# Kernel optimization log

Measured on AMD Instinct MI355X. Metric: run time of the kernel, lower is better.

The kernel has to match this reference:

```python
import jax, jax.numpy as jnp
import numpy as np

B, N, D, DFC, EMB, L = 16, 1024, 128, 128, 64, 4
NHOPS = (1, 2, 3, 4)  # tatic='cont': nhop(i) = i + 1
EDGE_P = 0.03


def _make_adj(k):
    u = jax.random.uniform(k, (B, N, N))
    a = u < EDGE_P
    a = a | jnp.transpose(a, (0, 2, 1))          # undirected
    a = a | jnp.eye(N, dtype=bool)[None]         # self loops
    return a.astype(jnp.float32)


def setup_inputs() -> dict:
    key = jax.random.key(0)
    ks = jax.random.split(key, 16)
    s = 0.05
    x = jax.random.normal(ks[0], (B, N, 2 * EMB), jnp.float32)
    adj1 = _make_adj(ks[1])
    adj2 = _make_adj(ks[2])
    valid = jnp.ones((B, N), jnp.float32)
    embede_w = jax.random.normal(ks[3], (D, 2 * EMB)) * s
    gW = jax.random.normal(ks[4], (L, D, D)) * s
    gb = jnp.zeros((L, D), jnp.float32)
    gA = jax.random.normal(ks[5], (L, D, D)) * s
    gate_w = jax.random.normal(ks[6], (L, 1, 2 * D)) * s
    gate_b = jnp.zeros((L, 1), jnp.float32)
    fc0_w = jax.random.normal(ks[7], (DFC, D)) * s
    fc0_b = jnp.zeros((DFC,), jnp.float32)
    fc1_w = jax.random.normal(ks[8], (DFC, DFC)) * s
    fc1_b = jnp.zeros((DFC,), jnp.float32)
    fc2_w = jax.random.normal(ks[9], (DFC, DFC)) * s
    fc2_b = jnp.zeros((DFC,), jnp.float32)
    fc3_w = jax.random.normal(ks[10], (1, DFC)) * s
    fc3_b = jnp.zeros((1,), jnp.float32)
    return dict(x=x, adj1=adj1, adj2=adj2, valid=valid, embede_w=embede_w,
                gW=gW, gb=gb, gA=gA, gate_w=gate_w, gate_b=gate_b,
                fc0_w=fc0_w, fc0_b=fc0_b, fc1_w=fc1_w, fc1_b=fc1_b,
                fc2_w=fc2_w, fc2_b=fc2_b, fc3_w=fc3_w, fc3_b=fc3_b)


def _glema(x, adj, W, b, A, gw, gbias, nhop):
    h = x @ W.T + b                                        # [B,N,D]
    e = jnp.einsum('bjl,bkl->bjk', jnp.einsum('bjd,de->bje', h, A), h)
    e = e + jnp.transpose(e, (0, 2, 1))                    # undirected
    att = jnp.where(adj > 0, e, jnp.float32(0.0))
    att = jax.nn.softmax(att, axis=1) * adj                # softmax over dim 1, then adj mask
    az = jax.nn.relu(jnp.einsum('bij,bjd->bid', att, h))
    coeff = jax.nn.sigmoid(jnp.concatenate([h, az], -1) @ gw.T + gbias)  # [B,N,1]
    z = h
    for _ in range(nhop):
        az = jax.nn.relu(jnp.einsum('bij,bjd->bid', att, z))
        z = coeff * h + (1.0 - coeff) * az
    return z


def reference(x, adj1, adj2, valid, embede_w, gW, gb, gA, gate_w, gate_b,
              fc0_w, fc0_b, fc1_w, fc1_b, fc2_w, fc2_b, fc3_w, fc3_b):
    h = x @ embede_w.T                                     # embede (no bias)
    for k in range(L):                                     # branch='both': c_hs2 - c_hs1
        h1 = _glema(h, adj1, gW[k], gb[k], gA[k], gate_w[k], gate_b[k], NHOPS[k])
        h2 = _glema(h, adj2, gW[k], gb[k], gA[k], gate_w[k], gate_b[k], NHOPS[k])
        h = h2 - h1                                        # dropout p used in eval mode -> identity
    h = h * valid[..., None]
    pooled = h.sum(1) / valid.sum(1, keepdims=True)        # [B,D]
    y = jax.nn.relu(pooled @ fc0_w.T + fc0_b)
    y = jax.nn.relu(y @ fc1_w.T + fc1_b)
    y = jax.nn.relu(y @ fc2_w.T + fc2_b)
    y = jax.nn.sigmoid(y @ fc3_w.T + fc3_b)
    return y.reshape(-1)                                   # [B]
```

## Files before the change

kernel.cpp:

```cpp
#include <hip/hip_runtime.h>

typedef _Float16 half_t;
typedef _Float16 half8 __attribute__((ext_vector_type(8)));
typedef _Float16 half4v __attribute__((ext_vector_type(4)));
typedef float floatx4 __attribute__((ext_vector_type(4)));

#define MFMA(a,b,c) __builtin_amdgcn_mfma_f32_16x16x32_f16(a,b,c,0,0,0)

#define NB 16
#define NLEN 1024
#define DD 128
#define BN (NB*NLEN)
#define BND ((size_t)NB*NLEN*DD)
#define BNN ((size_t)NB*NLEN*NLEN)
#define ELLS 128
#define EMP 1044

static __device__ inline half_t f16h(unsigned pk) {
    unsigned short us = (unsigned short)(pk & 0xffffu);
    half_t h; __builtin_memcpy(&h, &us, 2); return h;
}

__global__ __launch_bounds__(256, 8)
void k_pre(const float* __restrict__ adj1, const float* __restrict__ adj2,
           unsigned* __restrict__ ell, unsigned* __restrict__ cntA,
           const float* __restrict__ x, const float* __restrict__ Ew, half_t* __restrict__ h16,
           const float* __restrict__ gW, const float* __restrict__ gA,
           half_t* __restrict__ Wf, half_t* __restrict__ STf) {
    int tid = threadIdx.x;
    int bid = blockIdx.x;
    if (bid < 8192) {
        int w = tid >> 6, l = tid & 63;
        int R = bid * 4 + w;
        int br = R >> 14, nb = R & 16383;
        const float* arow = (br ? adj2 : adj1) + (size_t)nb * 1024;
        float4 v0 = *(const float4*)&arow[l * 4];
        float4 v1 = *(const float4*)&arow[256 + l * 4];
        float4 v2 = *(const float4*)&arow[512 + l * 4];
        float4 v3 = *(const float4*)&arow[768 + l * 4];
        unsigned m = 0u;
        m |= (v0.x > 0.f) ? 1u : 0u;        m |= (v0.y > 0.f) ? 2u : 0u;
        m |= (v0.z > 0.f) ? 4u : 0u;        m |= (v0.w > 0.f) ? 8u : 0u;
        m |= (v1.x > 0.f) ? 0x10u : 0u;     m |= (v1.y > 0.f) ? 0x20u : 0u;
        m |= (v1.z > 0.f) ? 0x40u : 0u;     m |= (v1.w > 0.f) ? 0x80u : 0u;
        m |= (v2.x > 0.f) ? 0x100u : 0u;    m |= (v2.y > 0.f) ? 0x200u : 0u;
        m |= (v2.z > 0.f) ? 0x400u : 0u;    m |= (v2.w > 0.f) ? 0x800u : 0u;
        m |= (v3.x > 0.f) ? 0x1000u : 0u;   m |= (v3.y > 0.f) ? 0x2000u : 0u;
        m |= (v3.z > 0.f) ? 0x4000u : 0u;   m |= (v3.w > 0.f) ? 0x8000u : 0u;
        int cnt = __popc(m);
        int pre = cnt;
#pragma unroll
        for (int off = 1; off < 64; off <<= 1) {
            int o = __shfl_up(pre, off);
            if (l >= off) pre += o;
        }
        int total = __shfl(pre, 63);
        int idx = pre - cnt;
        unsigned* erow = ell + (size_t)R * ELLS;
        unsigned mm = m;
        while (mm) {
            int i = __builtin_ctz(mm);
            mm &= mm - 1;
            if (idx < ELLS)
                erow[idx] = ((unsigned)(((i >> 2) << 8) + l * 4 + (i & 3))) << 16;
            idx++;
        }
        int cnc = total > ELLS ? ELLS : total;
        if (l == 0) cntA[R] = (unsigned)cnc;
        if (l < 4 && cnc + l < ELLS) erow[cnc + l] = 0u;
        return;
    }
    if (bid >= 10240) {
        int i = (bid - 10240) * 256 + tid;
        Wf[i] = (half_t)gW[i];
        int base = i & ~16383;
        int lrem = i & 16383;
        int d = lrem >> 7, e = lrem & 127;
        STf[base + (e << 7) + d] = (half_t)(gA[i] + gA[base + (e << 7) + d]);
        return;
    }
    __shared__ float rows[8][DD];
    int g = (bid - 8192) * 8;
    {
        int nl = tid >> 5, c4 = (tid & 31) * 4;
        *(float4*)&rows[nl][c4] = *(const float4*)&x[(size_t)(g + nl) * DD + c4];
    }
    __syncthreads();
    int t = tid & 127, half = tid >> 7;
    const float4* wr4 = (const float4*)(Ew + (size_t)t * DD);
    float acc[4] = {0.f, 0.f, 0.f, 0.f};
#pragma unroll 4
    for (int k4 = 0; k4 < 32; k4++) {
        float4 wv = wr4[k4];
#pragma unroll
        for (int mi = 0; mi < 4; mi++) {
            float4 rv = *(const float4*)&rows[half + 2 * mi][k4 * 4];
            acc[mi] += rv.x * wv.x + rv.y * wv.y + rv.z * wv.z + rv.w * wv.w;
        }
    }
#pragma unroll
    for (int mi = 0; mi < 4; mi++) h16[(size_t)(g + half + 2 * mi) * DD + t] = (half_t)acc[mi];
}

__global__ __launch_bounds__(256)
void k_proj(const half_t* __restrict__ pa, const half_t* __restrict__ pb,
            const half_t* __restrict__ Wf, const float* __restrict__ bias,
            const half_t* __restrict__ STf,
            half_t* __restrict__ hbr16, half_t* __restrict__ hbrF, half_t* __restrict__ hSF) {
    __shared__ half_t htile[32 * 136];
    __shared__ half_t hbtile[32 * 136];
    int g = blockIdx.x * 32;
    int t = threadIdx.x;
    int w = t >> 6, l = t & 63, q = l >> 4, l15 = l & 15;
#pragma unroll
    for (int v = 0; v < 2; v++) {
        int idx = v * 256 + t; int r = idx >> 4, c8 = (idx & 15) * 8;
        half8 va = *(const half8*)&pa[((size_t)(g + r) << 7) + c8];
        if (pb) {
            half8 vb = *(const half8*)&pb[((size_t)(g + r) << 7) + c8];
            va = va - vb;
        }
        *(half8*)&htile[r * 136 + c8] = va;
    }
    __syncthreads();
    int rowh = (w & 1) * 16;
    int c0 = (w >> 1) * 4;
    half8 a1[4];
#pragma unroll
    for (int kc = 0; kc < 4; kc++) a1[kc] = *(const half8*)&htile[(rowh + l15) * 136 + kc * 32 + q * 8];
    floatx4 acc[4];
#pragma unroll
    for (int cc = 0; cc < 4; cc++) {
        int col = (c0 + cc) * 16 + l15;
        floatx4 a = {0.f, 0.f, 0.f, 0.f};
#pragma unroll
        for (int kc = 0; kc < 4; kc++) {
            half8 bf = *(const half8*)&Wf[((size_t)col << 7) + kc * 32 + q * 8];
            a = MFMA(a1[kc], bf, a);
        }
        float bv = bias[col];
        a.x += bv; a.y += bv; a.z += bv; a.w += bv;
        acc[cc] = a;
    }
#pragma unroll
    for (int cc = 0; cc < 4; cc++) {
        int col = (c0 + cc) * 16 + l15;
#pragma unroll
        for (int r = 0; r < 4; r++)
            hbtile[(rowh + q * 4 + r) * 136 + col] = (half_t)acc[cc][r];
    }
    __syncthreads();
    half8 a2[4];
#pragma unroll
    for (int kc = 0; kc < 4; kc++) a2[kc] = *(const half8*)&hbtile[(rowh + l15) * 136 + kc * 32 + q * 8];
#pragma unroll
    for (int cc = 0; cc < 4; cc++) {
        int col = (c0 + cc) * 16 + l15;
        floatx4 a = {0.f, 0.f, 0.f, 0.f};
#pragma unroll
        for (int kc = 0; kc < 4; kc++) {
            half8 bf = *(const half8*)&STf[((size_t)col << 7) + kc * 32 + q * 8];
            a = MFMA(a2[kc], bf, a);
        }
        acc[cc] = a;
    }
    __syncthreads();
#pragma unroll
    for (int cc = 0; cc < 4; cc++) {
        int col = (c0 + cc) * 16 + l15;
#pragma unroll
        for (int r = 0; r < 4; r++) htile[(rowh + q * 4 + r) * 136 + col] = (half_t)acc[cc][r];
    }
    __syncthreads();
#pragma unroll
    for (int v = 0; v < 2; v++) {
        int idx = v * 256 + t; int r = idx >> 4, c8 = (idx & 15) * 8;
        *(half8*)&hbr16[((size_t)(g + r) << 7) + c8] = *(const half8*)&hbtile[r * 136 + c8];
    }
#pragma unroll
    for (int v = 0; v < 2; v++) {
        int fi = v * 256 + t;
        int g2 = fi >> 8, kc = (fi >> 6) & 3, li = fi & 63;
        int src = (g2 * 16 + (li & 15)) * 136 + kc * 32 + (li >> 4) * 8;
        size_t dst = (((size_t)(blockIdx.x * 2 + g2) * 4 + kc) << 10) + li * 8;
        *(half8*)&hbrF[dst] = *(const half8*)&hbtile[src];
        *(half8*)&hSF[dst]  = *(const half8*)&htile[src];
    }
}

__global__ __launch_bounds__(256)
void k_E(const half_t* __restrict__ hSF, const half_t* __restrict__ hbrF,
         const half_t* __restrict__ hbr16,
         unsigned* __restrict__ ell, const unsigned* __restrict__ cntA,
         float* __restrict__ rsr, half_t* __restrict__ hbrs) {
    int hw = blockIdx.y * 64 + blockIdx.x;
    int wk = (hw & 7) * 128 + (hw >> 3);
    int b = wk >> 6, s = wk & 63;
    int t = threadIdx.x, w = t >> 6, l = t & 63, q = l >> 4, l15 = l & 15;
    __shared__ half_t emS[16 * EMP];
    __shared__ float rsS[2][16];
    size_t Gb = (size_t)b * 64;
    half8 A[4];
#pragma unroll
    for (int kc = 0; kc < 4; kc++)
        A[kc] = *(const half8*)&hSF[(((Gb + s) * 4 + kc) << 10) + l * 8];
#pragma unroll 4
    for (int cg = 0; cg < 16; cg++) {
        int c0 = w * 256 + cg * 16;
        floatx4 a = {0.f, 0.f, 0.f, 0.f};
#pragma unroll
        for (int kc = 0; kc < 4; kc++) {
            half8 bf = *(const half8*)&hbrF[(((Gb + w * 16 + cg) * 4 + kc) << 10) + l * 8];
            a = MFMA(A[kc], bf, a);
        }
#pragma unroll
        for (int r = 0; r < 4; r++)
            emS[(q * 4 + r) * EMP + c0 + l15] = (half_t)a[r];
    }
    __syncthreads();
    const float CN = 0.000335462627903f;
#pragma unroll
    for (int rr = 0; rr < 4; rr++) {
        int rl = w * 4 + rr;
        int rowg = b * 1024 + s * 16 + rl;
#pragma unroll
        for (int br = 0; br < 2; br++) {
            size_t R = ((size_t)br << 14) + rowg;
            int cn = (int)cntA[R];
            float rs = 0.f;
            for (int base = 0; base < cn; base += 64) {
                int si = base + l;
                float v = 0.f;
                if (si < cn) {
                    unsigned pk = ell[R * ELLS + si];
                    int col = (int)(pk >> 16);
                    float em = (float)emS[rl * EMP + col];
                    v = __expf(em - 8.f);
                    half_t hv = (half_t)v;
                    unsigned short us; __builtin_memcpy(&us, &hv, 2);
                    ((unsigned short*)ell)[(R * ELLS + si) * 2] = us;
                }
                rs += v;
            }
            rs += __shfl_xor(rs, 1); rs += __shfl_xor(rs, 2);
            rs += __shfl_xor(rs, 4); rs += __shfl_xor(rs, 8);
            rs += __shfl_xor(rs, 16); rs += __shfl_xor(rs, 32);
            if (l == 0) {
                float rv = 1.f / (rs + (1024.f - (float)cn) * CN);
                rsr[R] = rv;
                rsS[br][rl] = rv;
            }
        }
    }
    __syncthreads();
    const half_t* hrow = hbr16 + ((size_t)b << 17) + ((size_t)(s * 16) << 7);
#pragma unroll
    for (int v = 0; v < 2; v++) {
        int idx = v * 256 + t;
        int row = idx >> 5, br2 = (idx >> 4) & 1, ch = idx & 15;
        half8 hv = *(const half8*)&hrow[(size_t)row * 128 + ch * 8];
        float sc = rsS[br2][row];
        half8 o;
#pragma unroll
        for (int d = 0; d < 8; d++) o[d] = (half_t)(sc * (float)hv[d]);
        *(half8*)&hbrs[(size_t)br2 * BND + ((size_t)(b * 1024 + s * 16 + row) << 7) + ch * 8] = o;
    }
}

__global__ __launch_bounds__(256)
void k_az(const unsigned* __restrict__ ell, const unsigned* __restrict__ cntA,
          const float* __restrict__ rsr,
          const half_t* __restrict__ zin, const half_t* __restrict__ hbr16,
          const float* __restrict__ gw, const float* __restrict__ gb_,
          float* __restrict__ cfb, half_t* __restrict__ outp, int mode) {
    int t = threadIdx.x, w = t >> 6, l = t & 63;
    int g = l >> 4, l15 = l & 15;
    int bid = blockIdx.x;
    int wk = (bid & 7) * 256 + (bid >> 3);
    int R = wk * 16 + w * 4 + g;
    int br = R >> 14, nb = R & 16383;
    const unsigned* ep = ell + (size_t)R * ELLS;
    int cn = (int)cntA[R];
    const half_t* zb = zin + (size_t)br * BND + (((size_t)(nb & ~1023)) << 7) + l15 * 8;
    half8 acc8a = {}, acc8b = {};
    uint4 p4 = *(const uint4*)ep;
    for (int s = 0; s < cn; s += 4) {
        uint4 cur = p4;
        p4 = *(const uint4*)(ep + s + 4);
        half8 z0 = *(const half8*)(zb + (((size_t)(cur.x >> 16)) << 7));
        half8 z1 = *(const half8*)(zb + (((size_t)(cur.y >> 16)) << 7));
        half8 z2 = *(const half8*)(zb + (((size_t)(cur.z >> 16)) << 7));
        half8 z3 = *(const half8*)(zb + (((size_t)(cur.w >> 16)) << 7));
        half_t h0 = f16h(cur.x), h1 = f16h(cur.y), h2 = f16h(cur.z), h3 = f16h(cur.w);
        half8 s0 = {h0,h0,h0,h0,h0,h0,h0,h0};
        half8 s1 = {h1,h1,h1,h1,h1,h1,h1,h1};
        half8 s2 = {h2,h2,h2,h2,h2,h2,h2,h2};
        half8 s3 = {h3,h3,h3,h3,h3,h3,h3,h3};
        acc8a += z0 * s0;
        acc8b += z1 * s1;
        acc8a += z2 * s2;
        acc8b += z3 * s3;
    }
    float acc[8];
#pragma unroll
    for (int d = 0; d < 8; d++) acc[d] = fmaxf((float)acc8a[d] + (float)acc8b[d], 0.f);
    half8 hv8 = *(const half8*)&hbr16[((size_t)nb << 7) + l15 * 8];
    float hv[8];
#pragma unroll
    for (int d = 0; d < 8; d++) hv[d] = (float)hv8[d];
    float cf;
    if (mode >= 3) {
        const float* g1 = gw + l15 * 8;
        const float* g2 = gw + 128 + l15 * 8;
        float dp = 0.f;
#pragma unroll
        for (int d = 0; d < 8; d++) dp += hv[d] * g1[d] + acc[d] * g2[d];
        dp += __shfl_xor(dp, 1); dp += __shfl_xor(dp, 2);
        dp += __shfl_xor(dp, 4); dp += __shfl_xor(dp, 8);
        cf = 1.f / (1.f + __expf(-(dp + gb_[0])));
        if (l15 == 0) cfb[R] = cf;
    } else {
        cf = cfb[R];
    }
    float sc = (mode == 1 || mode == 3) ? rsr[R] : 1.f;
    half8 o;
#pragma unroll
    for (int d = 0; d < 8; d++)
        o[d] = (half_t)(sc * (cf * hv[d] + (1.f - cf) * acc[d]));
    *(half8*)&outp[(size_t)R * DD + l15 * 8] = o;
}

__global__ __launch_bounds__(256)
void k_pool(const half_t* __restrict__ z2, const half_t* __restrict__ z1,
            const float* __restrict__ valid, float* __restrict__ part) {
    int b = blockIdx.y, s = blockIdx.x;
    int t = threadIdx.x, d = t & 127, hf = t >> 7;
    __shared__ float red[128];
    float acc = 0.f;
    int nbase = s * 128 + hf * 64;
    for (int n = nbase; n < nbase + 64; n++) {
        size_t gi = ((size_t)(b * 1024 + n) << 7) + d;
        acc += ((float)z2[gi] - (float)z1[gi]) * valid[b * 1024 + n];
    }
    if (hf) red[d] = acc;
    __syncthreads();
    if (!hf) part[(b * 8 + s) * 128 + d] = acc + red[d];
}

__global__ __launch_bounds__(128)
void k_mlp(const float* __restrict__ part, const float* __restrict__ valid,
           const float* __restrict__ w0, const float* __restrict__ b0,
           const float* __restrict__ w1, const float* __restrict__ b1,
           const float* __restrict__ w2, const float* __restrict__ b2,
           const float* __restrict__ w3, const float* __restrict__ b3,
           float* __restrict__ out) {
    int b = blockIdx.x, t = threadIdx.x;
    __shared__ float y0[DD], y1[DD];
    __shared__ float sred[2];
    float vs = 0.f;
    for (int n = t; n < NLEN; n += 128) vs += valid[b * NLEN + n];
    for (int off = 32; off; off >>= 1) vs += __shfl_down(vs, off);
    if ((t & 63) == 0) sred[t >> 6] = vs;
    __syncthreads();
    float vsum = sred[0] + sred[1];
    float acc = 0.f;
#pragma unroll
    for (int s = 0; s < 8; s++) acc += part[(b * 8 + s) * 128 + t];
    y0[t] = acc / vsum;
    __syncthreads();
    float a = b0[t];
    for (int k = 0; k < DD; k++) a += y0[k] * w0[t * DD + k];
    y1[t] = fmaxf(a, 0.f);
    __syncthreads();
    a = b1[t];
    for (int k = 0; k < DD; k++) a += y1[k] * w1[t * DD + k];
    y0[t] = fmaxf(a, 0.f);
    __syncthreads();
    a = b2[t];
    for (int k = 0; k < DD; k++) a += y0[k] * w2[t * DD + k];
    y1[t] = fmaxf(a, 0.f);
    __syncthreads();
    float p = y1[t] * w3[t];
    for (int off = 32; off; off >>= 1) p += __shfl_down(p, off);
    if ((t & 63) == 0) sred[t >> 6] = p;
    __syncthreads();
    if (t == 0) out[b] = 1.f / (1.f + __expf(-(sred[0] + sred[1] + b3[0])));
}

extern "C" void kernel_launch(void* const* d_in, const int* in_sizes, int n_in,
                              void* d_out, int out_size, void* d_ws, size_t ws_size,
                              hipStream_t stream) {
    (void)in_sizes; (void)n_in; (void)out_size; (void)ws_size;
    const float* x     = (const float*)d_in[0];
    const float* adj1  = (const float*)d_in[1];
    const float* adj2  = (const float*)d_in[2];
    const float* valid = (const float*)d_in[3];
    const float* Ew    = (const float*)d_in[4];
    const float* gW    = (const float*)d_in[5];
    const float* gb    = (const float*)d_in[6];
    const float* gA    = (const float*)d_in[7];
    const float* gatew = (const float*)d_in[8];
    const float* gateb = (const float*)d_in[9];
    const float* w0 = (const float*)d_in[10]; const float* b0 = (const float*)d_in[11];
    const float* w1 = (const float*)d_in[12]; const float* b1 = (const float*)d_in[13];
    const float* w2 = (const float*)d_in[14]; const float* b2 = (const float*)d_in[15];
    const float* w3 = (const float*)d_in[16]; const float* b3 = (const float*)d_in[17];
    float* out = (float*)d_out;

    char* p = (char*)d_ws;
    float* rsr  = (float*)p; p += 2 * BN * 4;
    float* cfb  = (float*)p; p += 2 * BN * 4;
    float* partb = (float*)p; p += (size_t)NB * 8 * 128 * 4;
    half_t* h16   = (half_t*)p; p += BND * 2;
    half_t* hbr16 = (half_t*)p; p += BND * 2;
    half_t* hbrF  = (half_t*)p; p += BND * 2;
    half_t* hSF   = (half_t*)p; p += BND * 2;
    half_t* hbrs  = (half_t*)p; p += 2 * BND * 2;
    half_t* zf    = (half_t*)p; p += 2 * BND * 2;
    half_t* zsA   = (half_t*)p; p += 2 * BND * 2;
    half_t* zsB   = (half_t*)p; p += 2 * BND * 2;
    unsigned* ell = (unsigned*)p; p += (size_t)2 * BN * ELLS * 4 + 16;
    unsigned* cntA = (unsigned*)p; p += (size_t)2 * BN * 4;
    half_t* Wf16 = (half_t*)p; p += (size_t)4 * 128 * 128 * 2;
    half_t* ST16 = (half_t*)p; p += (size_t)4 * 128 * 128 * 2;

    k_pre<<<10496, 256, 0, stream>>>(adj1, adj2, ell, cntA, x, Ew, h16, gW, gA, Wf16, ST16);

    for (int k = 0; k < 4; k++) {
        int nhop = k + 1;
        const half_t* pa = k ? (zf + BND) : h16;
        const half_t* pb = k ? zf : nullptr;
        k_proj<<<512, 256, 0, stream>>>(pa, pb, Wf16 + (size_t)k * 16384, gb + k * 128,
                                        ST16 + (size_t)k * 16384, hbr16, hbrF, hSF);
        k_E<<<dim3(64, NB), 256, 0, stream>>>(hSF, hbrF, hbr16, ell, cntA, rsr, hbrs);
        half_t* tgate = (nhop == 1) ? zf : zsA;
        k_az<<<2048, 256, 0, stream>>>(ell, cntA, rsr, hbrs, hbr16,
                                       gatew + k * 256, gateb + k, cfb, tgate,
                                       (nhop == 1) ? 4 : 3);
        half_t* src = tgate;
        for (int hop = 2; hop <= nhop; hop++) {
            half_t* dst = (hop == nhop) ? zf : ((hop & 1) ? zsA : zsB);
            k_az<<<2048, 256, 0, stream>>>(ell, cntA, rsr, src, hbr16,
                                           gatew + k * 256, gateb + k, cfb, dst,
                                           (hop == nhop) ? 2 : 1);
            src = dst;
        }
    }
    k_pool<<<dim3(8, NB), 256, 0, stream>>>(zf + BND, zf, valid, partb);
    k_mlp<<<16, 128, 0, stream>>>(partb, valid, w0, b0, w1, b1, w2, b2, w3, b3, out);
}
```

Baseline: 680.6 us.

## Split ELL neighbor lists by column half and stage Z slices in LDS for SpMM

The ELL build now partitions each row's neighbor list into low (cols <512) and high (cols >=512) segments, with padded offsets packed into cntA. k_az uses 512-thread blocks covering 128 rows of one graph. Each block loads the half of that graph's Z matrix (512x128 fp16, 128KB) into shared memory in two phases and gathers from LDS instead of global memory. This is meant to replace scattered global/L2 gathers with LDS reads. In exchange it uses far fewer blocks (256), needs very large shared memory, and caps each half's neighbor count.

```diff
diff --git a/kernel.cpp b/kernel.cpp
--- a/kernel.cpp
+++ b/kernel.cpp
@@ -12,7 +12,6 @@
 #define DD 128
 #define BN (NB*NLEN)
 #define BND ((size_t)NB*NLEN*DD)
-#define BNN ((size_t)NB*NLEN*NLEN)
 #define ELLS 128
 #define EMP 1044
 
@@ -47,27 +46,42 @@
         m |= (v2.z > 0.f) ? 0x400u : 0u;    m |= (v2.w > 0.f) ? 0x800u : 0u;
         m |= (v3.x > 0.f) ? 0x1000u : 0u;   m |= (v3.y > 0.f) ? 0x2000u : 0u;
         m |= (v3.z > 0.f) ? 0x4000u : 0u;   m |= (v3.w > 0.f) ? 0x8000u : 0u;
-        int cnt = __popc(m);
-        int pre = cnt;
+        unsigned m_lo = m & 0xFFu, m_hi = m >> 8;
+        int c_lo = __popc(m_lo), c_hi = __popc(m_hi);
+        int p_lo = c_lo, p_hi = c_hi;
 #pragma unroll
         for (int off = 1; off < 64; off <<= 1) {
-            int o = __shfl_up(pre, off);
-            if (l >= off) pre += o;
-        }
-        int total = __shfl(pre, 63);
-        int idx = pre - cnt;
+            int o1 = __shfl_up(p_lo, off);
+            int o2 = __shfl_up(p_hi, off);
+            if (l >= off) { p_lo += o1; p_hi += o2; }
+        }
+        int tot_lo = __shfl(p_lo, 63), tot_hi = __shfl(p_hi, 63);
+        int cl = tot_lo > 96 ? 96 : tot_lo;
+        int hs = (cl + 3) & ~3;
+        int chm = ELLS - 4 - hs;
+        int ch = tot_hi > chm ? chm : tot_hi;
         unsigned* erow = ell + (size_t)R * ELLS;
-        unsigned mm = m;
+        int idx = p_lo - c_lo;
+        unsigned mm = m_lo;
         while (mm) {
             int i = __builtin_ctz(mm);
             mm &= mm - 1;
-            if (idx < ELLS)
+            if (idx < cl)
                 erow[idx] = ((unsigned)(((i >> 2) << 8) + l * 4 + (i & 3))) << 16;
             idx++;
         }
-        int cnc = total > ELLS ? ELLS : total;
-        if (l == 0) cntA[R] = (unsigned)cnc;
-        if (l < 4 && cnc + l < ELLS) erow[cnc + l] = 0u;
+        int idxh = p_hi - c_hi;
+        mm = m_hi;
+        while (mm) {
+            int j = __builtin_ctz(mm);
+            mm &= mm - 1;
+            if (idxh < ch)
+                erow[hs + idxh] = ((unsigned)((((j >> 2) + 2) << 8) + l * 4 + (j & 3))) << 16;
+            idxh++;
+        }
+        if (l < hs - cl) erow[cl + l] = 0u;
+        if (l < 4 && hs + ch + l < ELLS) erow[hs + ch + l] = 0u;
+        if (l == 0) cntA[R] = (unsigned)cl | ((unsigned)hs << 8) | ((unsigned)ch << 16);
         return;
     }
     if (bid >= 10240) {
@@ -226,12 +240,13 @@
 #pragma unroll
         for (int br = 0; br < 2; br++) {
             size_t R = ((size_t)br << 14) + rowg;
-            int cn = (int)cntA[R];
+            unsigned cp = cntA[R];
+            int cl = (int)(cp & 255u), hs = (int)((cp >> 8) & 255u), ch = (int)((cp >> 16) & 255u);
             float rs = 0.f;
-            for (int base = 0; base < cn; base += 64) {
+            for (int base = 0; base < cl; base += 64) {
                 int si = base + l;
                 float v = 0.f;
-                if (si < cn) {
+                if (si < cl) {
                     unsigned pk = ell[R * ELLS + si];
                     int col = (int)(pk >> 16);
                     float em = (float)emS[rl * EMP + col];
@@ -242,11 +257,25 @@
                 }
                 rs += v;
             }
+            for (int base = 0; base < ch; base += 64) {
+                int si = base + l;
+                float v = 0.f;
+                if (si < ch) {
+                    unsigned pk = ell[R * ELLS + hs + si];
+                    int col = (int)(pk >> 16);
+                    float em = (float)emS[rl * EMP + col];
+                    v = __expf(em - 8.f);
+                    half_t hv = (half_t)v;
+                    unsigned short us; __builtin_memcpy(&us, &hv, 2);
+                    ((unsigned short*)ell)[(R * ELLS + hs + si) * 2] = us;
+                }
+                rs += v;
+            }
             rs += __shfl_xor(rs, 1); rs += __shfl_xor(rs, 2);
             rs += __shfl_xor(rs, 4); rs += __shfl_xor(rs, 8);
             rs += __shfl_xor(rs, 16); rs += __shfl_xor(rs, 32);
             if (l == 0) {
-                float rv = 1.f / (rs + (1024.f - (float)cn) * CN);
+                float rv = 1.f / (rs + (1024.f - (float)(cl + ch)) * CN);
                 rsr[R] = rv;
                 rsS[br][rl] = rv;
             }
@@ -257,77 +286,100 @@
 #pragma unroll
     for (int v = 0; v < 2; v++) {
         int idx = v * 256 + t;
-        int row = idx >> 5, br2 = (idx >> 4) & 1, ch = idx & 15;
-        half8 hv = *(const half8*)&hrow[(size_t)row * 128 + ch * 8];
+        int row = idx >> 5, br2 = (idx >> 4) & 1, ch2 = idx & 15;
+        half8 hv = *(const half8*)&hrow[(size_t)row * 128 + ch2 * 8];
         float sc = rsS[br2][row];
         half8 o;
 #pragma unroll
         for (int d = 0; d < 8; d++) o[d] = (half_t)(sc * (float)hv[d]);
-        *(half8*)&hbrs[(size_t)br2 * BND + ((size_t)(b * 1024 + s * 16 + row) << 7) + ch * 8] = o;
-    }
-}
-
-__global__ __launch_bounds__(256)
+        *(half8*)&hbrs[(size_t)br2 * BND + ((size_t)(b * 1024 + s * 16 + row) << 7) + ch2 * 8] = o;
+    }
+}
+
+__global__ __launch_bounds__(512)
 void k_az(const unsigned* __restrict__ ell, const unsigned* __restrict__ cntA,
           const float* __restrict__ rsr,
           const half_t* __restrict__ zin, const half_t* __restrict__ hbr16,
           const float* __restrict__ gw, const float* __restrict__ gb_,
           float* __restrict__ cfb, half_t* __restrict__ outp, int mode) {
+    __shared__ half_t zS[512 * 128];
     int t = threadIdx.x, w = t >> 6, l = t & 63;
     int g = l >> 4, l15 = l & 15;
     int bid = blockIdx.x;
-    int wk = (bid & 7) * 256 + (bid >> 3);
-    int R = wk * 16 + w * 4 + g;
-    int br = R >> 14, nb = R & 16383;
-    const unsigned* ep = ell + (size_t)R * ELLS;
-    int cn = (int)cntA[R];
-    const half_t* zb = zin + (size_t)br * BND + (((size_t)(nb & ~1023)) << 7) + l15 * 8;
-    half8 acc8a = {}, acc8b = {};
-    uint4 p4 = *(const uint4*)ep;
-    for (int s = 0; s < cn; s += 4) {
-        uint4 cur = p4;
-        p4 = *(const uint4*)(ep + s + 4);
-        half8 z0 = *(const half8*)(zb + (((size_t)(cur.x >> 16)) << 7));
-        half8 z1 = *(const half8*)(zb + (((size_t)(cur.y >> 16)) << 7));
-        half8 z2 = *(const half8*)(zb + (((size_t)(cur.z >> 16)) << 7));
-        half8 z3 = *(const half8*)(zb + (((size_t)(cur.w >> 16)) << 7));
-        half_t h0 = f16h(cur.x), h1 = f16h(cur.y), h2 = f16h(cur.z), h3 = f16h(cur.w);
-        half8 s0 = {h0,h0,h0,h0,h0,h0,h0,h0};
-        half8 s1 = {h1,h1,h1,h1,h1,h1,h1,h1};
-        half8 s2 = {h2,h2,h2,h2,h2,h2,h2,h2};
-        half8 s3 = {h3,h3,h3,h3,h3,h3,h3,h3};
-        acc8a += z0 * s0;
-        acc8b += z1 * s1;
-        acc8a += z2 * s2;
-        acc8b += z3 * s3;
-    }
-    float acc[8];
-#pragma unroll
-    for (int d = 0; d < 8; d++) acc[d] = fmaxf((float)acc8a[d] + (float)acc8b[d], 0.f);
-    half8 hv8 = *(const half8*)&hbr16[((size_t)nb << 7) + l15 * 8];
-    float hv[8];
-#pragma unroll
-    for (int d = 0; d < 8; d++) hv[d] = (float)hv8[d];
-    float cf;
-    if (mode >= 3) {
-        const float* g1 = gw + l15 * 8;
-        const float* g2 = gw + 128 + l15 * 8;
-        float dp = 0.f;
-#pragma unroll
-        for (int d = 0; d < 8; d++) dp += hv[d] * g1[d] + acc[d] * g2[d];
-        dp += __shfl_xor(dp, 1); dp += __shfl_xor(dp, 2);
-        dp += __shfl_xor(dp, 4); dp += __shfl_xor(dp, 8);
-        cf = 1.f / (1.f + __expf(-(dp + gb_[0])));
-        if (l15 == 0) cfb[R] = cf;
-    } else {
-        cf = cfb[R];
-    }
-    float sc = (mode == 1 || mode == 3) ? rsr[R] : 1.f;
-    half8 o;
-#pragma unroll
-    for (int d = 0; d < 8; d++)
-        o[d] = (half_t)(sc * (cf * hv[d] + (1.f - cf) * acc[d]));
-    *(half8*)&outp[(size_t)R * DD + l15 * 8] = o;
+    int xcd = bid & 7, chunk = (bid >> 3) & 7, slot = bid >> 6;
+    int p = slot * 8 + xcd;
+    int br = p & 1, b = p >> 1;
+    int Rbase = br * 16384 + b * 1024 + chunk * 128;
+    const half_t* zslice = zin + (size_t)br * BND + ((size_t)(b * 1024) << 7);
+    half8 accA[4] = {}, accB[4] = {};
+    for (int ph = 0; ph < 2; ph++) {
+        __syncthreads();
+        const half_t* src = zslice + ((size_t)(ph * 512) << 7);
+        for (int i = 0; i < 16; i++) {
+            int idx = i * 512 + t;
+            *(half8*)&zS[idx * 8] = *(const half8*)&src[idx * 8];
+        }
+        __syncthreads();
+#pragma unroll
+        for (int it = 0; it < 4; it++) {
+            int R = Rbase + it * 32 + w * 4 + g;
+            unsigned cp = cntA[R];
+            int cl = (int)(cp & 255u), hs = (int)((cp >> 8) & 255u), ch = (int)((cp >> 16) & 255u);
+            int s0 = ph ? hs : 0;
+            int cn = ph ? ch : cl;
+            const unsigned* ep = ell + (size_t)R * ELLS + s0;
+            uint4 nxt = *(const uint4*)ep;
+            for (int s = 0; s < cn; s += 4) {
+                uint4 cur = nxt;
+                nxt = *(const uint4*)(ep + s + 4);
+                half8 z0 = *(const half8*)&zS[(size_t)((cur.x >> 16) & 511) * 128 + l15 * 8];
+                half8 z1 = *(const half8*)&zS[(size_t)((cur.y >> 16) & 511) * 128 + l15 * 8];
+                half8 z2 = *(const half8*)&zS[(size_t)((cur.z >> 16) & 511) * 128 + l15 * 8];
+                half8 z3 = *(const half8*)&zS[(size_t)((cur.w >> 16) & 511) * 128 + l15 * 8];
+                half_t h0 = f16h(cur.x), h1 = f16h(cur.y), h2 = f16h(cur.z), h3 = f16h(cur.w);
+                half8 s0v = {h0,h0,h0,h0,h0,h0,h0,h0};
+                half8 s1v = {h1,h1,h1,h1,h1,h1,h1,h1};
+                half8 s2v = {h2,h2,h2,h2,h2,h2,h2,h2};
+                half8 s3v = {h3,h3,h3,h3,h3,h3,h3,h3};
+                accA[it] += z0 * s0v;
+                accB[it] += z1 * s1v;
+                accA[it] += z2 * s2v;
+                accB[it] += z3 * s3v;
+            }
+        }
+    }
+#pragma unroll
+    for (int it = 0; it < 4; it++) {
+        int R = Rbase + it * 32 + w * 4 + g;
+        int nb = R & 16383;
+        float acc[8];
+#pragma unroll
+        for (int d = 0; d < 8; d++) acc[d] = fmaxf((float)accA[it][d] + (float)accB[it][d], 0.f);
+        half8 hv8 = *(const half8*)&hbr16[((size_t)nb << 7) + l15 * 8];
+        float hv[8];
+#pragma unroll
+        for (int d = 0; d < 8; d++) hv[d] = (float)hv8[d];
+        float cf;
+        if (mode >= 3) {
+            const float* g1 = gw + l15 * 8;
+            const float* g2 = gw + 128 + l15 * 8;
+            float dp = 0.f;
+#pragma unroll
+            for (int d = 0; d < 8; d++) dp += hv[d] * g1[d] + acc[d] * g2[d];
+            dp += __shfl_xor(dp, 1); dp += __shfl_xor(dp, 2);
+            dp += __shfl_xor(dp, 4); dp += __shfl_xor(dp, 8);
+            cf = 1.f / (1.f + __expf(-(dp + gb_[0])));
+            if (l15 == 0) cfb[R] = cf;
+        } else {
+            cf = cfb[R];
+        }
+        float sc = (mode == 1 || mode == 3) ? rsr[R] : 1.f;
+        half8 o;
+#pragma unroll
+        for (int d = 0; d < 8; d++)
+            o[d] = (half_t)(sc * (cf * hv[d] + (1.f - cf) * acc[d]));
+        *(half8*)&outp[(size_t)R * DD + l15 * 8] = o;
+    }
 }
 
 __global__ __launch_bounds__(256)
@@ -380,9 +432,9 @@
     for (int k = 0; k < DD; k++) a += y0[k] * w2[t * DD + k];
     y1[t] = fmaxf(a, 0.f);
     __syncthreads();
-    float p = y1[t] * w3[t];
-    for (int off = 32; off; off >>= 1) p += __shfl_down(p, off);
-    if ((t & 63) == 0) sred[t >> 6] = p;
+    float pv = y1[t] * w3[t];
+    for (int off = 32; off; off >>= 1) pv += __shfl_down(pv, off);
+    if ((t & 63) == 0) sred[t >> 6] = pv;
     __syncthreads();
     if (t == 0) out[b] = 1.f / (1.f + __expf(-(sred[0] + sred[1] + b3[0])));
 }
@@ -434,15 +486,15 @@
                                         ST16 + (size_t)k * 16384, hbr16, hbrF, hSF);
         k_E<<<dim3(64, NB), 256, 0, stream>>>(hSF, hbrF, hbr16, ell, cntA, rsr, hbrs);
         half_t* tgate = (nhop == 1) ? zf : zsA;
-        k_az<<<2048, 256, 0, stream>>>(ell, cntA, rsr, hbrs, hbr16,
-                                       gatew + k * 256, gateb + k, cfb, tgate,
-                                       (nhop == 1) ? 4 : 3);
+        k_az<<<256, 512, 0, stream>>>(ell, cntA, rsr, hbrs, hbr16,
+                                      gatew + k * 256, gateb + k, cfb, tgate,
+                                      (nhop == 1) ? 4 : 3);
         half_t* src = tgate;
         for (int hop = 2; hop <= nhop; hop++) {
             half_t* dst = (hop == nhop) ? zf : ((hop & 1) ? zsA : zsB);
-            k_az<<<2048, 256, 0, stream>>>(ell, cntA, rsr, src, hbr16,
-                                           gatew + k * 256, gateb + k, cfb, dst,
-                                           (hop == nhop) ? 2 : 1);
+            k_az<<<256, 512, 0, stream>>>(ell, cntA, rsr, src, hbr16,
+                                          gatew + k * 256, gateb + k, cfb, dst,
+                                          (hop == nhop) ? 2 : 1);
             src = dst;
         }
     }
```

Result: slower. 717.3 us (+5.4%).

## Replace ELL sparse gather aggregation with dense masked-attention MFMA GEMM

Applied to the files above, without the earlier changes.

Drops the ELL sparse neighbor lists and instead stores a 16-bit adjacency bitmask per 16 columns. k_E writes a dense fp16 masked exp-attention matrix Dm, and a new k_azd kernel computes each hop's aggregation as a dense 1024x1024 by 1024x128 MFMA GEMM. Intermediate z is kept in transposed layout so it can feed the B operand directly. This removes irregular gathers and the ELL truncation at 128 neighbors, but does about 30x more arithmetic on a ~6% dense matrix and adds 64MB of Dm traffic per layer, with A/B operands loaded straight from global memory with no LDS tiling.

```diff
diff --git a/kernel.cpp b/kernel.cpp
--- a/kernel.cpp
+++ b/kernel.cpp
@@ -2,7 +2,6 @@
 
 typedef _Float16 half_t;
 typedef _Float16 half8 __attribute__((ext_vector_type(8)));
-typedef _Float16 half4v __attribute__((ext_vector_type(4)));
 typedef float floatx4 __attribute__((ext_vector_type(4)));
 
 #define MFMA(a,b,c) __builtin_amdgcn_mfma_f32_16x16x32_f16(a,b,c,0,0,0)
@@ -12,18 +11,11 @@
 #define DD 128
 #define BN (NB*NLEN)
 #define BND ((size_t)NB*NLEN*DD)
-#define BNN ((size_t)NB*NLEN*NLEN)
-#define ELLS 128
 #define EMP 1044
-
-static __device__ inline half_t f16h(unsigned pk) {
-    unsigned short us = (unsigned short)(pk & 0xffffu);
-    half_t h; __builtin_memcpy(&h, &us, 2); return h;
-}
 
 __global__ __launch_bounds__(256, 8)
 void k_pre(const float* __restrict__ adj1, const float* __restrict__ adj2,
-           unsigned* __restrict__ ell, unsigned* __restrict__ cntA,
+           unsigned short* __restrict__ mask16,
            const float* __restrict__ x, const float* __restrict__ Ew, half_t* __restrict__ h16,
            const float* __restrict__ gW, const float* __restrict__ gA,
            half_t* __restrict__ Wf, half_t* __restrict__ STf) {
@@ -33,41 +25,17 @@
         int w = tid >> 6, l = tid & 63;
         int R = bid * 4 + w;
         int br = R >> 14, nb = R & 16383;
-        const float* arow = (br ? adj2 : adj1) + (size_t)nb * 1024;
-        float4 v0 = *(const float4*)&arow[l * 4];
-        float4 v1 = *(const float4*)&arow[256 + l * 4];
-        float4 v2 = *(const float4*)&arow[512 + l * 4];
-        float4 v3 = *(const float4*)&arow[768 + l * 4];
+        const float* arow = (br ? adj2 : adj1) + (size_t)nb * 1024 + l * 16;
         unsigned m = 0u;
-        m |= (v0.x > 0.f) ? 1u : 0u;        m |= (v0.y > 0.f) ? 2u : 0u;
-        m |= (v0.z > 0.f) ? 4u : 0u;        m |= (v0.w > 0.f) ? 8u : 0u;
-        m |= (v1.x > 0.f) ? 0x10u : 0u;     m |= (v1.y > 0.f) ? 0x20u : 0u;
-        m |= (v1.z > 0.f) ? 0x40u : 0u;     m |= (v1.w > 0.f) ? 0x80u : 0u;
-        m |= (v2.x > 0.f) ? 0x100u : 0u;    m |= (v2.y > 0.f) ? 0x200u : 0u;
-        m |= (v2.z > 0.f) ? 0x400u : 0u;    m |= (v2.w > 0.f) ? 0x800u : 0u;
-        m |= (v3.x > 0.f) ? 0x1000u : 0u;   m |= (v3.y > 0.f) ? 0x2000u : 0u;
-        m |= (v3.z > 0.f) ? 0x4000u : 0u;   m |= (v3.w > 0.f) ? 0x8000u : 0u;
-        int cnt = __popc(m);
-        int pre = cnt;
-#pragma unroll
-        for (int off = 1; off < 64; off <<= 1) {
-            int o = __shfl_up(pre, off);
-            if (l >= off) pre += o;
-        }
-        int total = __shfl(pre, 63);
-        int idx = pre - cnt;
-        unsigned* erow = ell + (size_t)R * ELLS;
-        unsigned mm = m;
-        while (mm) {
-            int i = __builtin_ctz(mm);
-            mm &= mm - 1;
-            if (idx < ELLS)
-                erow[idx] = ((unsigned)(((i >> 2) << 8) + l * 4 + (i & 3))) << 16;
-            idx++;
-        }
-        int cnc = total > ELLS ? ELLS : total;
-        if (l == 0) cntA[R] = (unsigned)cnc;
-        if (l < 4 && cnc + l < ELLS) erow[cnc + l] = 0u;
+#pragma unroll
+        for (int c = 0; c < 4; c++) {
+            float4 v = *(const float4*)&arow[c * 4];
+            m |= (v.x > 0.f ? 1u : 0u) << (c * 4);
+            m |= (v.y > 0.f ? 1u : 0u) << (c * 4 + 1);
+            m |= (v.z > 0.f ? 1u : 0u) << (c * 4 + 2);
+            m |= (v.w > 0.f ? 1u : 0u) << (c * 4 + 3);
+        }
+        mask16[(size_t)R * 64 + l] = (unsigned short)m;
         return;
     }
     if (bid >= 10240) {
@@ -106,7 +74,8 @@
 void k_proj(const half_t* __restrict__ pa, const half_t* __restrict__ pb,
             const half_t* __restrict__ Wf, const float* __restrict__ bias,
             const half_t* __restrict__ STf,
-            half_t* __restrict__ hbr16, half_t* __restrict__ hbrF, half_t* __restrict__ hSF) {
+            half_t* __restrict__ hbr16, half_t* __restrict__ hbrT,
+            half_t* __restrict__ hbrF, half_t* __restrict__ hSF) {
     __shared__ half_t htile[32 * 136];
     __shared__ half_t hbtile[32 * 136];
     int g = blockIdx.x * 32;
@@ -176,6 +145,19 @@
     for (int v = 0; v < 2; v++) {
         int idx = v * 256 + t; int r = idx >> 4, c8 = (idx & 15) * 8;
         *(half8*)&hbr16[((size_t)(g + r) << 7) + c8] = *(const half8*)&hbtile[r * 136 + c8];
+    }
+    {
+        int b_ = g >> 10, gi = g & 1023;
+        int d = t >> 1, hh = t & 1;
+        half8 r0, r1;
+#pragma unroll
+        for (int e = 0; e < 8; e++) {
+            r0[e] = hbtile[(hh * 16 + e) * 136 + d];
+            r1[e] = hbtile[(hh * 16 + 8 + e) * 136 + d];
+        }
+        half_t* op = hbrT + ((size_t)b_ * 128 + d) * 1024 + gi + hh * 16;
+        *(half8*)op = r0;
+        *(half8*)(op + 8) = r1;
     }
 #pragma unroll
     for (int v = 0; v < 2; v++) {
@@ -190,9 +172,8 @@
 
 __global__ __launch_bounds__(256)
 void k_E(const half_t* __restrict__ hSF, const half_t* __restrict__ hbrF,
-         const half_t* __restrict__ hbr16,
-         unsigned* __restrict__ ell, const unsigned* __restrict__ cntA,
-         float* __restrict__ rsr, half_t* __restrict__ hbrs) {
+         const unsigned short* __restrict__ mask16, const half_t* __restrict__ hbrT,
+         half_t* __restrict__ Dm, float* __restrict__ rsr, half_t* __restrict__ hbrsT) {
     int hw = blockIdx.y * 64 + blockIdx.x;
     int wk = (hw & 7) * 128 + (hw >> 3);
     int b = wk >> 6, s = wk & 63;
@@ -220,114 +201,165 @@
     __syncthreads();
     const float CN = 0.000335462627903f;
 #pragma unroll
-    for (int rr = 0; rr < 4; rr++) {
-        int rl = w * 4 + rr;
-        int rowg = b * 1024 + s * 16 + rl;
-#pragma unroll
-        for (int br = 0; br < 2; br++) {
-            size_t R = ((size_t)br << 14) + rowg;
-            int cn = (int)cntA[R];
-            float rs = 0.f;
-            for (int base = 0; base < cn; base += 64) {
-                int si = base + l;
-                float v = 0.f;
-                if (si < cn) {
-                    unsigned pk = ell[R * ELLS + si];
-                    int col = (int)(pk >> 16);
-                    float em = (float)emS[rl * EMP + col];
-                    v = __expf(em - 8.f);
-                    half_t hv = (half_t)v;
-                    unsigned short us; __builtin_memcpy(&us, &hv, 2);
-                    ((unsigned short*)ell)[(R * ELLS + si) * 2] = us;
-                }
-                rs += v;
+    for (int tt = 0; tt < 8; tt++) {
+        int task = tt * 4 + w;
+        int rl = task >> 1, br = task & 1;
+        size_t R = ((size_t)br << 14) + (size_t)b * 1024 + s * 16 + rl;
+        unsigned mv = (unsigned)mask16[R * 64 + l];
+        half8 e0 = *(const half8*)&emS[rl * EMP + l * 16];
+        half8 e1 = *(const half8*)&emS[rl * EMP + l * 16 + 8];
+        half8 o0, o1;
+        float rs = 0.f;
+#pragma unroll
+        for (int c2 = 0; c2 < 8; c2++) {
+            float v0 = ((mv >> c2) & 1u) ? __expf((float)e0[c2] - 8.f) : 0.f;
+            float v1 = ((mv >> (c2 + 8)) & 1u) ? __expf((float)e1[c2] - 8.f) : 0.f;
+            o0[c2] = (half_t)v0; o1[c2] = (half_t)v1;
+            rs += v0 + v1;
+        }
+        *(half8*)&Dm[R * 1024 + l * 16] = o0;
+        *(half8*)&Dm[R * 1024 + l * 16 + 8] = o1;
+        int cn = __popc(mv);
+        rs += __shfl_xor(rs, 1); rs += __shfl_xor(rs, 2);
+        rs += __shfl_xor(rs, 4); rs += __shfl_xor(rs, 8);
+        rs += __shfl_xor(rs, 16); rs += __shfl_xor(rs, 32);
+        cn += __shfl_xor(cn, 1); cn += __shfl_xor(cn, 2);
+        cn += __shfl_xor(cn, 4); cn += __shfl_xor(cn, 8);
+        cn += __shfl_xor(cn, 16); cn += __shfl_xor(cn, 32);
+        if (l == 0) {
+            float rv = 1.f / (rs + (1024.f - (float)cn) * CN);
+            rsr[R] = rv;
+            rsS[br][rl] = rv;
+        }
+    }
+    __syncthreads();
+    {
+        int d = t >> 1, br = t & 1;
+        const half_t* hp = hbrT + ((size_t)b * 128 + d) * 1024 + s * 16;
+        half8 a0 = *(const half8*)hp, a1 = *(const half8*)(hp + 8);
+        half8 r0, r1;
+#pragma unroll
+        for (int e = 0; e < 8; e++) {
+            r0[e] = (half_t)((float)a0[e] * rsS[br][e]);
+            r1[e] = (half_t)((float)a1[e] * rsS[br][8 + e]);
+        }
+        half_t* op = hbrsT + (((size_t)((br << 4) + b)) * 128 + d) * 1024 + s * 16;
+        *(half8*)op = r0;
+        *(half8*)(op + 8) = r1;
+    }
+}
+
+__global__ __launch_bounds__(256)
+void k_azd(const half_t* __restrict__ Dm, const float* __restrict__ rsr,
+           const half_t* __restrict__ BT, const half_t* __restrict__ hbr16,
+           const float* __restrict__ gw, const float* __restrict__ gb_,
+           float* __restrict__ cfb, half_t* __restrict__ outR, half_t* __restrict__ outT,
+           int mode) {
+    __shared__ half_t azS[128 * 136];
+    int t = threadIdx.x, w = t >> 6, l = t & 63, q = l >> 4, l15 = l & 15;
+    int bid = blockIdx.x;
+    int xcd = bid & 7, mm = bid >> 3;
+    int slice = xcd * 4 + (mm >> 3), tile = mm & 7;
+    int br = slice & 1, b = slice >> 1;
+    int c = (br << 4) + b;
+    const half_t* Dp = Dm + ((size_t)c << 20);
+    const half_t* Bp = BT + ((size_t)c << 17);
+    int i0 = tile * 128 + w * 32;
+    const half_t* Ar0 = Dp + (size_t)(i0 + l15) * 1024 + q * 8;
+    const half_t* Ar1 = Dp + (size_t)(i0 + 16 + l15) * 1024 + q * 8;
+    const half_t* Brow = Bp + (size_t)l15 * 1024 + q * 8;
+    floatx4 acc[2][8] = {};
+    half8 a0[2], b0v[8], a1[2], b1v[8];
+    a0[0] = *(const half8*)Ar0;
+    a0[1] = *(const half8*)Ar1;
+#pragma unroll
+    for (int nf = 0; nf < 8; nf++) b0v[nf] = *(const half8*)(Brow + nf * 16384);
+    for (int kc = 0; kc < 32; kc += 2) {
+        int k1 = (kc + 1) * 32, k2 = ((kc + 2) & 31) * 32;
+        a1[0] = *(const half8*)(Ar0 + k1);
+        a1[1] = *(const half8*)(Ar1 + k1);
+#pragma unroll
+        for (int nf = 0; nf < 8; nf++) b1v[nf] = *(const half8*)(Brow + nf * 16384 + k1);
+#pragma unroll
+        for (int nf = 0; nf < 8; nf++) {
+            acc[0][nf] = MFMA(a0[0], b0v[nf], acc[0][nf]);
+            acc[1][nf] = MFMA(a0[1], b0v[nf], acc[1][nf]);
+        }
+        a0[0] = *(const half8*)(Ar0 + k2);
+        a0[1] = *(const half8*)(Ar1 + k2);
+#pragma unroll
+        for (int nf = 0; nf < 8; nf++) b0v[nf] = *(const half8*)(Brow + nf * 16384 + k2);
+#pragma unroll
+        for (int nf = 0; nf < 8; nf++) {
+            acc[0][nf] = MFMA(a1[0], b1v[nf], acc[0][nf]);
+            acc[1][nf] = MFMA(a1[1], b1v[nf], acc[1][nf]);
+        }
+    }
+#pragma unroll
+    for (int mf = 0; mf < 2; mf++)
+#pragma unroll
+        for (int nf = 0; nf < 8; nf++)
+#pragma unroll
+            for (int r = 0; r < 4; r++)
+                azS[(w * 32 + mf * 16 + q * 4 + r) * 136 + nf * 16 + l15] = (half_t)acc[mf][nf][r];
+    __syncthreads();
+#pragma unroll
+    for (int it = 0; it < 8; it++) {
+        int iloc = it * 16 + w * 4 + q;
+        int i = tile * 128 + iloc;
+        int nb = b * 1024 + i;
+        int R = c * 1024 + i;
+        half8 az8 = *(const half8*)&azS[iloc * 136 + l15 * 8];
+        half8 hv8 = *(const half8*)&hbr16[((size_t)nb << 7) + l15 * 8];
+        float av[8], hv[8];
+#pragma unroll
+        for (int d = 0; d < 8; d++) {
+            av[d] = fmaxf((float)az8[d], 0.f);
+            hv[d] = (float)hv8[d];
+        }
+        float cf;
+        if (mode >= 3) {
+            const float* g1 = gw + l15 * 8;
+            const float* g2 = gw + 128 + l15 * 8;
+            float dp = 0.f;
+#pragma unroll
+            for (int d = 0; d < 8; d++) dp += hv[d] * g1[d] + av[d] * g2[d];
+            dp += __shfl_xor(dp, 1); dp += __shfl_xor(dp, 2);
+            dp += __shfl_xor(dp, 4); dp += __shfl_xor(dp, 8);
+            cf = 1.f / (1.f + __expf(-(dp + gb_[0])));
+            if (l15 == 0) cfb[R] = cf;
+        } else {
+            cf = cfb[R];
+        }
+        if (mode == 2 || mode == 4) {
+            half8 o;
+#pragma unroll
+            for (int d = 0; d < 8; d++) o[d] = (half_t)(cf * hv[d] + (1.f - cf) * av[d]);
+            *(half8*)&outR[(size_t)R * DD + l15 * 8] = o;
+        } else {
+            float sc = rsr[R];
+#pragma unroll
+            for (int d = 0; d < 8; d++)
+                azS[iloc * 136 + l15 * 8 + d] = (half_t)(sc * (cf * hv[d] + (1.f - cf) * av[d]));
+        }
+    }
+    if (mode == 1 || mode == 3) {
+        __syncthreads();
+        int d = t >> 1, hh = t & 1;
+#pragma unroll
+        for (int c2 = 0; c2 < 4; c2++) {
+            int ic = hh * 64 + c2 * 16;
+            half8 r0, r1;
+#pragma unroll
+            for (int e = 0; e < 8; e++) {
+                r0[e] = azS[(ic + e) * 136 + d];
+                r1[e] = azS[(ic + 8 + e) * 136 + d];
             }
-            rs += __shfl_xor(rs, 1); rs += __shfl_xor(rs, 2);
-            rs += __shfl_xor(rs, 4); rs += __shfl_xor(rs, 8);
-            rs += __shfl_xor(rs, 16); rs += __shfl_xor(rs, 32);
-            if (l == 0) {
-                float rv = 1.f / (rs + (1024.f - (float)cn) * CN);
-                rsr[R] = rv;
-                rsS[br][rl] = rv;
-            }
-        }
-    }
-    __syncthreads();
-    const half_t* hrow = hbr16 + ((size_t)b << 17) + ((size_t)(s * 16) << 7);
-#pragma unroll
-    for (int v = 0; v < 2; v++) {
-        int idx = v * 256 + t;
-        int row = idx >> 5, br2 = (idx >> 4) & 1, ch = idx & 15;
-        half8 hv = *(const half8*)&hrow[(size_t)row * 128 + ch * 8];
-        float sc = rsS[br2][row];
-        half8 o;
-#pragma unroll
-        for (int d = 0; d < 8; d++) o[d] = (half_t)(sc * (float)hv[d]);
-        *(half8*)&hbrs[(size_t)br2 * BND + ((size_t)(b * 1024 + s * 16 + row) << 7) + ch * 8] = o;
-    }
-}
-
-__global__ __launch_bounds__(256)
-void k_az(const unsigned* __restrict__ ell, const unsigned* __restrict__ cntA,
-          const float* __restrict__ rsr,
-          const half_t* __restrict__ zin, const half_t* __restrict__ hbr16,
-          const float* __restrict__ gw, const float* __restrict__ gb_,
-          float* __restrict__ cfb, half_t* __restrict__ outp, int mode) {
-    int t = threadIdx.x, w = t >> 6, l = t & 63;
-    int g = l >> 4, l15 = l & 15;
-    int bid = blockIdx.x;
-    int wk = (bid & 7) * 256 + (bid >> 3);
-    int R = wk * 16 + w * 4 + g;
-    int br = R >> 14, nb = R & 16383;
-    const unsigned* ep = ell + (size_t)R * ELLS;
-    int cn = (int)cntA[R];
-    const half_t* zb = zin + (size_t)br * BND + (((size_t)(nb & ~1023)) << 7) + l15 * 8;
-    half8 acc8a = {}, acc8b = {};
-    uint4 p4 = *(const uint4*)ep;
-    for (int s = 0; s < cn; s += 4) {
-        uint4 cur = p4;
-        p4 = *(const uint4*)(ep + s + 4);
-        half8 z0 = *(const half8*)(zb + (((size_t)(cur.x >> 16)) << 7));
-        half8 z1 = *(const half8*)(zb + (((size_t)(cur.y >> 16)) << 7));
-        half8 z2 = *(const half8*)(zb + (((size_t)(cur.z >> 16)) << 7));
-        half8 z3 = *(const half8*)(zb + (((size_t)(cur.w >> 16)) << 7));
-        half_t h0 = f16h(cur.x), h1 = f16h(cur.y), h2 = f16h(cur.z), h3 = f16h(cur.w);
-        half8 s0 = {h0,h0,h0,h0,h0,h0,h0,h0};
-        half8 s1 = {h1,h1,h1,h1,h1,h1,h1,h1};
-        half8 s2 = {h2,h2,h2,h2,h2,h2,h2,h2};
-        half8 s3 = {h3,h3,h3,h3,h3,h3,h3,h3};
-        acc8a += z0 * s0;
-        acc8b += z1 * s1;
-        acc8a += z2 * s2;
-        acc8b += z3 * s3;
-    }
-    float acc[8];
-#pragma unroll
-    for (int d = 0; d < 8; d++) acc[d] = fmaxf((float)acc8a[d] + (float)acc8b[d], 0.f);
-    half8 hv8 = *(const half8*)&hbr16[((size_t)nb << 7) + l15 * 8];
-    float hv[8];
-#pragma unroll
-    for (int d = 0; d < 8; d++) hv[d] = (float)hv8[d];
-    float cf;
-    if (mode >= 3) {
-        const float* g1 = gw + l15 * 8;
-        const float* g2 = gw + 128 + l15 * 8;
-        float dp = 0.f;
-#pragma unroll
-        for (int d = 0; d < 8; d++) dp += hv[d] * g1[d] + acc[d] * g2[d];
-        dp += __shfl_xor(dp, 1); dp += __shfl_xor(dp, 2);
-        dp += __shfl_xor(dp, 4); dp += __shfl_xor(dp, 8);
-        cf = 1.f / (1.f + __expf(-(dp + gb_[0])));
-        if (l15 == 0) cfb[R] = cf;
-    } else {
-        cf = cfb[R];
-    }
-    float sc = (mode == 1 || mode == 3) ? rsr[R] : 1.f;
-    half8 o;
-#pragma unroll
-    for (int d = 0; d < 8; d++)
-        o[d] = (half_t)(sc * (cf * hv[d] + (1.f - cf) * acc[d]));
-    *(half8*)&outp[(size_t)R * DD + l15 * 8] = o;
+            half_t* op = outT + ((size_t)c * 128 + d) * 1024 + tile * 128 + ic;
+            *(half8*)op = r0;
+            *(half8*)(op + 8) = r1;
+        }
+    }
 }
 
 __global__ __launch_bounds__(256)
@@ -380,9 +412,9 @@
     for (int k = 0; k < DD; k++) a += y0[k] * w2[t * DD + k];
     y1[t] = fmaxf(a, 0.f);
     __syncthreads();
-    float p = y1[t] * w3[t];
-    for (int off = 32; off; off >>= 1) p += __shfl_down(p, off);
-    if ((t & 63) == 0) sred[t >> 6] = p;
+    float pv = y1[t] * w3[t];
+    for (int off = 32; off; off >>= 1) pv += __shfl_down(pv, off);
+    if ((t & 63) == 0) sred[t >> 6] = pv;
     __syncthreads();
     if (t == 0) out[b] = 1.f / (1.f + __expf(-(sred[0] + sred[1] + b3[0])));
 }
@@ -415,35 +447,43 @@
     half_t* hbr16 = (half_t*)p; p += BND * 2;
     half_t* hbrF  = (half_t*)p; p += BND * 2;
     half_t* hSF   = (half_t*)p; p += BND * 2;
-    half_t* hbrs  = (half_t*)p; p += 2 * BND * 2;
+    half_t* hbrT  = (half_t*)p; p += BND * 2;
+    half_t* hbrsT = (half_t*)p; p += 2 * BND * 2;
     half_t* zf    = (half_t*)p; p += 2 * BND * 2;
-    half_t* zsA   = (half_t*)p; p += 2 * BND * 2;
-    half_t* zsB   = (half_t*)p; p += 2 * BND * 2;
-    unsigned* ell = (unsigned*)p; p += (size_t)2 * BN * ELLS * 4 + 16;
-    unsigned* cntA = (unsigned*)p; p += (size_t)2 * BN * 4;
+    half_t* zTA   = (half_t*)p; p += 2 * BND * 2;
+    half_t* zTB   = (half_t*)p; p += 2 * BND * 2;
+    unsigned short* mask16 = (unsigned short*)p; p += (size_t)2 * BN * 64 * 2;
+    half_t* Dm   = (half_t*)p; p += (size_t)2 * BN * 1024 * 2;
     half_t* Wf16 = (half_t*)p; p += (size_t)4 * 128 * 128 * 2;
     half_t* ST16 = (half_t*)p; p += (size_t)4 * 128 * 128 * 2;
 
-    k_pre<<<10496, 256, 0, stream>>>(adj1, adj2, ell, cntA, x, Ew, h16, gW, gA, Wf16, ST16);
+    k_pre<<<10496, 256, 0, stream>>>(adj1, adj2, mask16, x, Ew, h16, gW, gA, Wf16, ST16);
 
     for (int k = 0; k < 4; k++) {
         int nhop = k + 1;
         const half_t* pa = k ? (zf + BND) : h16;
         const half_t* pb = k ? zf : nullptr;
         k_proj<<<512, 256, 0, stream>>>(pa, pb, Wf16 + (size_t)k * 16384, gb + k * 128,
-                                        ST16 + (size_t)k * 16384, hbr16, hbrF, hSF);
-        k_E<<<dim3(64, NB), 256, 0, stream>>>(hSF, hbrF, hbr16, ell, cntA, rsr, hbrs);
-        half_t* tgate = (nhop == 1) ? zf : zsA;
-        k_az<<<2048, 256, 0, stream>>>(ell, cntA, rsr, hbrs, hbr16,
-                                       gatew + k * 256, gateb + k, cfb, tgate,
-                                       (nhop == 1) ? 4 : 3);
-        half_t* src = tgate;
+                                        ST16 + (size_t)k * 16384, hbr16, hbrT, hbrF, hSF);
+        k_E<<<dim3(64, NB), 256, 0, stream>>>(hSF, hbrF, mask16, hbrT, Dm, rsr, hbrsT);
+        if (nhop == 1) {
+            k_azd<<<256, 256, 0, stream>>>(Dm, rsr, hbrsT, hbr16, gatew + k * 256, gateb + k,
+                                           cfb, zf, (half_t*)nullptr, 4);
+        } else {
+            k_azd<<<256, 256, 0, stream>>>(Dm, rsr, hbrsT, hbr16, gatew + k * 256, gateb + k,
+                                           cfb, (half_t*)nullptr, zTA, 3);
+        }
+        const half_t* srcT = zTA;
         for (int hop = 2; hop <= nhop; hop++) {
-            half_t* dst = (hop == nhop) ? zf : ((hop & 1) ? zsA : zsB);
-            k_az<<<2048, 256, 0, stream>>>(ell, cntA, rsr, src, hbr16,
-                                           gatew + k * 256, gateb + k, cfb, dst,
-                                           (hop == nhop) ? 2 : 1);
-            src = dst;
+            if (hop == nhop) {
+                k_azd<<<256, 256, 0, stream>>>(Dm, rsr, srcT, hbr16, gatew + k * 256, gateb + k,
+                                               cfb, zf, (half_t*)nullptr, 2);
+            } else {
+                half_t* dT = (hop & 1) ? zTA : zTB;
+                k_azd<<<256, 256, 0, stream>>>(Dm, rsr, srcT, hbr16, gatew + k * 256, gateb + k,
+                                               cfb, (half_t*)nullptr, dT, 1);
+                srcT = dT;
+            }
         }
     }
     k_pool<<<dim3(8, NB), 256, 0, stream>>>(zf + BND, zf, valid, partb);
```

After: 873.0 us. +28.3%, slower.
